# Kernel tuning notes

Hardware: AMD Instinct MI355X
Metric: run time of the kernel (lower is better)

Reference implementation:

```python
import jax, jax.numpy as jnp
import numpy as np

C_IN = 12      # total channels (rgb-noised + hidden)
C_NOISE = 3    # noise-prediction channels
HID = 128      # rule-MLP hidden size
PERC = 48      # perception channels (depthwise, 48/12 = 4 filters per channel)
TDIM = 256     # sinusoidal time-embedding dim


def setup_inputs() -> dict:
    key = jax.random.key(0)
    ks = jax.random.split(key, 12)
    B, H, W = 16, 256, 256
    x = jax.random.normal(ks[0], (B, C_NOISE, H, W), jnp.float32)
    hidden_channels = jax.random.normal(ks[1], (B, C_IN - C_NOISE, H, W), jnp.float32)
    t = jax.random.randint(ks[2], (B,), 0, 1000)
    # depthwise 3x3 perceive conv: torch weight shape [out=48, in/groups=1, 3, 3]
    w_perceive = jax.random.normal(ks[3], (PERC, 1, 3, 3), jnp.float32) * 0.1
    b_perceive = jax.random.normal(ks[4], (PERC,), jnp.float32) * 0.01
    # 1x1 convs of the rule network, stored as [out, in]
    w1 = jax.random.normal(ks[5], (HID, PERC), jnp.float32) * 0.1
    b1 = jax.random.normal(ks[6], (HID,), jnp.float32) * 0.01
    w2 = jax.random.normal(ks[7], (HID, HID), jnp.float32) * 0.05
    b2 = jax.random.normal(ks[8], (HID,), jnp.float32) * 0.01
    # conv3 is zero-initialized in the original; random here for test coverage
    w3 = jax.random.normal(ks[9], (C_IN, HID), jnp.float32) * 0.05
    # time embedding Linear(256 -> c_noise)
    w_time = jax.random.normal(ks[10], (C_NOISE, TDIM), jnp.float32) * 0.1
    b_time = jax.random.normal(ks[11], (C_NOISE,), jnp.float32) * 0.01
    return dict(x=x, hidden_channels=hidden_channels, t=t,
                w_perceive=w_perceive, b_perceive=b_perceive,
                w1=w1, b1=b1, w2=w2, b2=b2, w3=w3,
                w_time=w_time, b_time=b_time)


def _pos_encoding(t, channels):
    # t: [B] int -> [B, channels] sinusoidal embedding (torch repeat-then-scale layout)
    inv_freq = 1.0 / (10000.0 ** (jnp.arange(0, channels, 2, dtype=jnp.float32) / channels))
    ang = t.astype(jnp.float32)[:, None] * inv_freq  # [B, channels//2]
    return jnp.concatenate([jnp.sin(ang), jnp.cos(ang)], axis=-1)


def reference(x, hidden_channels, t, w_perceive, b_perceive, w1, b1, w2, b2, w3, w_time, b_time):
    # concat noised channels with hidden state channels -> [B, 12, H, W]
    xf = jnp.concatenate([x, hidden_channels], axis=1)
    # depthwise 3x3 conv, 'same' padding, groups = C_IN
    perc = jax.lax.conv_general_dilated(
        xf, w_perceive, window_strides=(1, 1), padding='SAME',
        feature_group_count=C_IN,
        dimension_numbers=('NCHW', 'OIHW', 'NCHW')) + b_perceive[None, :, None, None]
    # rule network: three 1x1 convs (pointwise MLP) with ReLUs
    h = jax.nn.relu(jnp.einsum('bchw,oc->bohw', perc, w1) + b1[None, :, None, None])
    h = jax.nn.relu(jnp.einsum('bchw,oc->bohw', h, w2) + b2[None, :, None, None])
    out = jnp.einsum('bchw,oc->bohw', h, w3)  # no bias
    # time embedding: sinusoidal -> SiLU -> Linear -> broadcast over H, W
    pe = _pos_encoding(t, TDIM)                       # [B, 256]
    emb = jax.nn.silu(pe) @ w_time.T + b_time         # [B, 3]
    noise_prediction = out[:, :C_NOISE] + emb[:, :, None, None]
    hidden_out = out[:, C_NOISE:]
    return (hidden_out, noise_prediction)
```

## Files before the change

### kernel.cpp

```cpp
#include <hip/hip_runtime.h>


#define ACT_S 136
#define PERC_S 72
#define NOISE_BASE 9437184

#define WSF_OFF 13312
#define WSF_BP 0
#define WSF_B1 48
#define WSF_B2 176
#define WSF_WP 304
#define WSF_EMB 736

typedef short bf16x8 __attribute__((ext_vector_type(8)));
typedef float f32x4 __attribute__((ext_vector_type(4)));

__device__ __forceinline__ short f2bf(float f) {
    union { float f; unsigned u; } cv; cv.f = f;
    unsigned r = cv.u + 0x7FFFu + ((cv.u >> 16) & 1u);
    return (short)(r >> 16);
}
__device__ __forceinline__ unsigned pk2bf(float f0, float f1) {
    union { float f; unsigned u; } a, b; a.f = f0; b.f = f1;
    return __builtin_amdgcn_perm(b.u + 0x8000u, a.u + 0x8000u, 0x07060302u);
}

__global__ void prep_emb_kernel(const float* __restrict__ wpg, const float* __restrict__ bpg,
                                const float* __restrict__ w1g, const float* __restrict__ b1g,
                                const float* __restrict__ w2g, const float* __restrict__ b2g,
                                const float* __restrict__ w3g,
                                const int* __restrict__ t,
                                const float* __restrict__ wt, const float* __restrict__ bt,
                                short* __restrict__ wsb, float* __restrict__ wsf)
{
    if (blockIdx.x < 107) {
        int i = blockIdx.x * 256 + threadIdx.x;
        if (i < 8192) {
            int o = i >> 6, c = i & 63;
            wsb[i] = (c < 48) ? f2bf(w1g[o * 48 + c]) : (short)0;
        } else if (i < 24576) {
            wsb[i] = f2bf(w2g[i - 8192]);
        } else if (i < 26624) {
            int k = i - 24576;
            wsb[i] = (k < 1536) ? f2bf(w3g[k]) : (short)0;
        } else if (i < 26672) {
            wsf[WSF_BP + (i - 26624)] = bpg[i - 26624];
        } else if (i < 26800) {
            wsf[WSF_B1 + (i - 26672)] = b1g[i - 26672];
        } else if (i < 26928) {
            wsf[WSF_B2 + (i - 26800)] = b2g[i - 26800];
        } else if (i < 27360) {
            wsf[WSF_WP + (i - 26928)] = wpg[i - 26928];
        }
        return;
    }
    int b = blockIdx.x - 107;
    int lane = threadIdx.x;
    if (lane >= 64) return;
    float tv = (float)t[b];
    float s0 = 0.f, s1 = 0.f, s2 = 0.f;
    const float LOG1E4 = 9.210340371976184f;
    #pragma unroll
    for (int ii = 0; ii < 2; ++ii) {
        int i = lane + ii * 64;
        float invf = __expf(-LOG1E4 * (float)i * (1.0f / 128.0f));
        float ang = tv * invf;
        float sn = sinf(ang), cs = cosf(ang);
        float ss = sn / (1.0f + __expf(-sn));
        float sc = cs / (1.0f + __expf(-cs));
        s0 += ss * wt[0 * 256 + i] + sc * wt[0 * 256 + i + 128];
        s1 += ss * wt[1 * 256 + i] + sc * wt[1 * 256 + i + 128];
        s2 += ss * wt[2 * 256 + i] + sc * wt[2 * 256 + i + 128];
    }
    #pragma unroll
    for (int off = 32; off; off >>= 1) {
        s0 += __shfl_down(s0, off);
        s1 += __shfl_down(s1, off);
        s2 += __shfl_down(s2, off);
    }
    if (lane == 0) {
        wsf[WSF_EMB + b * 3 + 0] = s0 + bt[0];
        wsf[WSF_EMB + b * 3 + 1] = s1 + bt[1];
        wsf[WSF_EMB + b * 3 + 2] = s2 + bt[2];
    }
}

__global__ __launch_bounds__(256, 3) void canet_main(
    const float* __restrict__ xg,
    const float* __restrict__ hg,
    const short* __restrict__ wsb,
    const float* __restrict__ wsf,
    float* __restrict__ outg)
{
    __shared__ __align__(16) short percS[64 * PERC_S];
    __shared__ __align__(16) short h1S[64 * ACT_S];
    __shared__ __align__(16) short h2S[64 * ACT_S];
    __shared__ __align__(16) float wp_s[48 * 12];
    __shared__ float bp_s[48];

    const int tid = threadIdx.x;
    const int b = blockIdx.x >> 8;
    const int y = blockIdx.x & 255;

    for (int i = tid; i < 576; i += 256) {
        int oc = i / 12, k = i % 12;
        wp_s[i] = (k < 9) ? wsf[WSF_WP + oc * 9 + k] : 0.0f;
    }
    if (tid < 48) bp_s[tid] = wsf[WSF_BP + tid];

    const int wv = tid >> 6;
    const int lane = tid & 63;
    const int m = lane & 15;
    const int q = lane >> 4;

    bf16x8 w1f[2][2], w2f[2][4], w3f[4];
    #pragma unroll
    for (int j = 0; j < 2; ++j) {
        int n = wv * 32 + j * 16 + m;
        #pragma unroll
        for (int ks = 0; ks < 2; ++ks)
            w1f[j][ks] = *(const bf16x8*)(wsb + n * 64 + ks * 32 + q * 8);
        #pragma unroll
        for (int ks = 0; ks < 4; ++ks)
            w2f[j][ks] = *(const bf16x8*)(wsb + 8192 + n * 128 + ks * 32 + q * 8);
    }
    #pragma unroll
    for (int ks = 0; ks < 4; ++ks)
        w3f[ks] = *(const bf16x8*)(wsb + 24576 + m * 128 + ks * 32 + q * 8);

    f32x4 b1v[2], b2v[2];
    #pragma unroll
    for (int j = 0; j < 2; ++j) {
        b1v[j] = *(const f32x4*)(wsf + WSF_B1 + wv * 32 + j * 16 + q * 4);
        b2v[j] = *(const f32x4*)(wsf + WSF_B2 + wv * 32 + j * 16 + q * 4);
    }
    const float embv = (m < 3) ? wsf[WSF_EMB + b * 3 + m] : 0.0f;

    const float* src3[3];
    #pragma unroll
    for (int i3 = 0; i3 < 3; ++i3) {
        int ic = 3 * q + i3;
        src3[i3] = (ic < 3) ? (xg + (((size_t)b * 3 + ic) << 16))
                            : (hg + (((size_t)b * 9 + (ic - 3)) << 16));
    }

    __syncthreads();

    for (int it = 0; it < 4; ++it) {
        const int x0 = it * 64;
        const int px = x0 + wv * 16 + m;

        {
            const int xm1 = px - (px > 0);
            const int xp1 = px + (px < 255);
            const bool okl = (px > 0), okr = (px < 255);
            short* prow = percS + (wv * 16 + m) * PERC_S;
            const bool interior = (y >= 1) && (y <= 254);
            #pragma unroll
            for (int i3 = 0; i3 < 3; ++i3) {
                const float* s = src3[i3];
                float tap[9];
                if (interior) {
                    #pragma unroll
                    for (int ky = 0; ky < 3; ++ky) {
                        const float* rp = s + (y + ky - 1) * 256;
                        float c0 = rp[xm1], c1 = rp[px], c2 = rp[xp1];
                        tap[ky * 3 + 0] = okl ? c0 : 0.0f;
                        tap[ky * 3 + 1] = c1;
                        tap[ky * 3 + 2] = okr ? c2 : 0.0f;
                    }
                } else {
                    #pragma unroll
                    for (int ky = 0; ky < 3; ++ky) {
                        int yy = y + ky - 1;
                        bool yok = (yy >= 0) && (yy < 256);
                        const float* rp = s + (yok ? yy : y) * 256;
                        float c0 = rp[xm1], c1 = rp[px], c2 = rp[xp1];
                        tap[ky * 3 + 0] = (yok && okl) ? c0 : 0.0f;
                        tap[ky * 3 + 1] = yok ? c1 : 0.0f;
                        tap[ky * 3 + 2] = (yok && okr) ? c2 : 0.0f;
                    }
                }
                float v[4];
                #pragma unroll
                for (int r = 0; r < 4; ++r) {
                    int oc = 12 * q + 4 * i3 + r;
                    const float* wrow = &wp_s[oc * 12];
                    f32x4 w0 = *(const f32x4*)wrow;
                    f32x4 w1_ = *(const f32x4*)(wrow + 4);
                    float a = bp_s[oc];
                    a += w0[0] * tap[0] + w0[1] * tap[1] + w0[2] * tap[2] + w0[3] * tap[3];
                    a += w1_[0] * tap[4] + w1_[1] * tap[5] + w1_[2] * tap[6] + w1_[3] * tap[7];
                    a += wrow[8] * tap[8];
                    v[r] = a;
                }
                uint2 pk;
                pk.x = pk2bf(v[0], v[1]);
                pk.y = pk2bf(v[2], v[3]);
                *(uint2*)(prow + 12 * q + 4 * i3) = pk;
            }
            *(uint2*)(prow + 48 + 4 * q) = uint2{0u, 0u};
        }
        __syncthreads();

        #pragma unroll
        for (int nt = 0; nt < 4; ++nt) {
            f32x4 c0 = b1v[0], c1 = b1v[1];
            #pragma unroll
            for (int ks = 0; ks < 2; ++ks) {
                bf16x8 p = *(const bf16x8*)(percS + (nt * 16 + m) * PERC_S + ks * 32 + q * 8);
                c0 = __builtin_amdgcn_mfma_f32_16x16x32_bf16(w1f[0][ks], p, c0, 0, 0, 0);
                c1 = __builtin_amdgcn_mfma_f32_16x16x32_bf16(w1f[1][ks], p, c1, 0, 0, 0);
            }
            short* drow = h1S + (nt * 16 + m) * ACT_S + wv * 32 + q * 4;
            uint2 pk;
            pk.x = pk2bf(fmaxf(c0[0], 0.f), fmaxf(c0[1], 0.f));
            pk.y = pk2bf(fmaxf(c0[2], 0.f), fmaxf(c0[3], 0.f));
            *(uint2*)drow = pk;
            pk.x = pk2bf(fmaxf(c1[0], 0.f), fmaxf(c1[1], 0.f));
            pk.y = pk2bf(fmaxf(c1[2], 0.f), fmaxf(c1[3], 0.f));
            *(uint2*)(drow + 16) = pk;
        }
        __syncthreads();

        #pragma unroll
        for (int nt = 0; nt < 4; ++nt) {
            f32x4 c0 = b2v[0], c1 = b2v[1];
            #pragma unroll
            for (int ks = 0; ks < 4; ++ks) {
                bf16x8 a = *(const bf16x8*)(h1S + (nt * 16 + m) * ACT_S + ks * 32 + q * 8);
                c0 = __builtin_amdgcn_mfma_f32_16x16x32_bf16(w2f[0][ks], a, c0, 0, 0, 0);
                c1 = __builtin_amdgcn_mfma_f32_16x16x32_bf16(w2f[1][ks], a, c1, 0, 0, 0);
            }
            short* drow = h2S + (nt * 16 + m) * ACT_S + wv * 32 + q * 4;
            uint2 pk;
            pk.x = pk2bf(fmaxf(c0[0], 0.f), fmaxf(c0[1], 0.f));
            pk.y = pk2bf(fmaxf(c0[2], 0.f), fmaxf(c0[3], 0.f));
            *(uint2*)drow = pk;
            pk.x = pk2bf(fmaxf(c1[0], 0.f), fmaxf(c1[1], 0.f));
            pk.y = pk2bf(fmaxf(c1[2], 0.f), fmaxf(c1[3], 0.f));
            *(uint2*)(drow + 16) = pk;
        }
        __syncthreads();

        {
            f32x4 acc = {0.f, 0.f, 0.f, 0.f};
            #pragma unroll
            for (int ks = 0; ks < 4; ++ks) {
                bf16x8 a = *(const bf16x8*)(h2S + (wv * 16 + m) * ACT_S + ks * 32 + q * 8);
                acc = __builtin_amdgcn_mfma_f32_16x16x32_bf16(a, w3f[ks], acc, 0, 0, 0);
            }
            if (m < 12) {
                int xx0 = x0 + wv * 16 + q * 4;
                size_t idx;
                if (m < 3) {
                    idx = (size_t)NOISE_BASE + (((size_t)b * 3 + m) << 16) + (size_t)y * 256 + xx0;
                } else {
                    idx = (((size_t)b * 9 + (m - 3)) << 16) + (size_t)y * 256 + xx0;
                }
                f32x4 vst = {acc[0] + embv, acc[1] + embv, acc[2] + embv, acc[3] + embv};
                *(f32x4*)(outg + idx) = vst;
            }
        }
    }
}

extern "C" void kernel_launch(void* const* d_in, const int* in_sizes, int n_in,
                              void* d_out, int out_size, void* d_ws, size_t ws_size,
                              hipStream_t stream) {
    const float* xg  = (const float*)d_in[0];
    const float* hg  = (const float*)d_in[1];
    const int*   tg  = (const int*)  d_in[2];
    const float* wpg = (const float*)d_in[3];
    const float* bpg = (const float*)d_in[4];
    const float* w1g = (const float*)d_in[5];
    const float* b1g = (const float*)d_in[6];
    const float* w2g = (const float*)d_in[7];
    const float* b2g = (const float*)d_in[8];
    const float* w3g = (const float*)d_in[9];
    const float* wtg = (const float*)d_in[10];
    const float* btg = (const float*)d_in[11];
    float* outg = (float*)d_out;
    short* wsb  = (short*)d_ws;
    float* wsf  = (float*)d_ws + WSF_OFF;

    prep_emb_kernel<<<123, 256, 0, stream>>>(wpg, bpg, w1g, b1g, w2g, b2g, w3g,
                                             tg, wtg, btg, wsb, wsf);
    canet_main<<<4096, 256, 0, stream>>>(xg, hg, wsb, wsf, outg);
}
```

Measured before the change: 226.8 us.

## Fold depthwise perceive conv into first MLP layer as MFMA over staged input taps

Precomputes a fused weight (w1 composed with the depthwise 3x3 filter) and fused bias in the prep kernel, so the first MLP layer becomes a K=144 (padded to 160) MFMA directly over a bf16 shared-memory tile of three input rows. This removes the per-pixel scalar FMA perception stage and its extra barrier, and loads the input rows once per block with coalesced float4 reads instead of scattered global taps. w2/w3 are now converted to bf16 inside the main kernel, block-to-row mapping is swizzled, and occupancy hint drops from 3 to 2 blocks. The cost is bf16 rounding of raw inputs, more MFMA work for layer 1, and larger LDS use.

```diff
diff --git a/kernel.cpp b/kernel.cpp
--- a/kernel.cpp
+++ b/kernel.cpp
@@ -2,15 +2,12 @@
 
 
 #define ACT_S 136
-#define PERC_S 72
+#define IN_ROW 4128
 #define NOISE_BASE 9437184
 
-#define WSF_OFF 13312
-#define WSF_BP 0
-#define WSF_B1 48
-#define WSF_B2 176
-#define WSF_WP 304
-#define WSF_EMB 736
+#define WSF_OFF 10240
+#define WSF_B1 0
+#define WSF_EMB 128
 
 typedef short bf16x8 __attribute__((ext_vector_type(8)));
 typedef float f32x4 __attribute__((ext_vector_type(4)));
@@ -20,41 +17,50 @@
     unsigned r = cv.u + 0x7FFFu + ((cv.u >> 16) & 1u);
     return (short)(r >> 16);
 }
+__device__ __forceinline__ short f2bf_fast(float f) {
+    union { float f; unsigned u; } cv; cv.f = f;
+    return (short)((cv.u + 0x8000u) >> 16);
+}
 __device__ __forceinline__ unsigned pk2bf(float f0, float f1) {
     union { float f; unsigned u; } a, b; a.f = f0; b.f = f1;
     return __builtin_amdgcn_perm(b.u + 0x8000u, a.u + 0x8000u, 0x07060302u);
 }
+__device__ __forceinline__ bf16x8 pk8bf(f32x4 a, f32x4 b) {
+    union { unsigned u[4]; bf16x8 v; } r;
+    r.u[0] = pk2bf(a[0], a[1]);
+    r.u[1] = pk2bf(a[2], a[3]);
+    r.u[2] = pk2bf(b[0], b[1]);
+    r.u[3] = pk2bf(b[2], b[3]);
+    return r.v;
+}
 
 __global__ void prep_emb_kernel(const float* __restrict__ wpg, const float* __restrict__ bpg,
                                 const float* __restrict__ w1g, const float* __restrict__ b1g,
-                                const float* __restrict__ w2g, const float* __restrict__ b2g,
-                                const float* __restrict__ w3g,
                                 const int* __restrict__ t,
                                 const float* __restrict__ wt, const float* __restrict__ bt,
                                 short* __restrict__ wsb, float* __restrict__ wsf)
 {
-    if (blockIdx.x < 107) {
+    if (blockIdx.x < 81) {
         int i = blockIdx.x * 256 + threadIdx.x;
-        if (i < 8192) {
-            int o = i >> 6, c = i & 63;
-            wsb[i] = (c < 48) ? f2bf(w1g[o * 48 + c]) : (short)0;
-        } else if (i < 24576) {
-            wsb[i] = f2bf(w2g[i - 8192]);
-        } else if (i < 26624) {
-            int k = i - 24576;
-            wsb[i] = (k < 1536) ? f2bf(w3g[k]) : (short)0;
-        } else if (i < 26672) {
-            wsf[WSF_BP + (i - 26624)] = bpg[i - 26624];
-        } else if (i < 26800) {
-            wsf[WSF_B1 + (i - 26672)] = b1g[i - 26672];
-        } else if (i < 26928) {
-            wsf[WSF_B2 + (i - 26800)] = b2g[i - 26800];
-        } else if (i < 27360) {
-            wsf[WSF_WP + (i - 26928)] = wpg[i - 26928];
+        if (i < 20480) {
+            int o = i / 160, k = i - o * 160;
+            int tp = k >> 4, icp = k & 15;
+            float val = 0.0f;
+            if (tp < 9 && icp < 12) {
+                #pragma unroll
+                for (int r = 0; r < 4; ++r)
+                    val += w1g[o * 48 + icp * 4 + r] * wpg[(icp * 4 + r) * 9 + tp];
+            }
+            wsb[i] = f2bf(val);
+        } else if (i < 20608) {
+            int o = i - 20480;
+            float v = b1g[o];
+            for (int oc = 0; oc < 48; ++oc) v += w1g[o * 48 + oc] * bpg[oc];
+            wsf[WSF_B1 + o] = v;
         }
         return;
     }
-    int b = blockIdx.x - 107;
+    int b = blockIdx.x - 81;
     int lane = threadIdx.x;
     if (lane >= 64) return;
     float tv = (float)t[b];
@@ -85,134 +91,119 @@
     }
 }
 
-__global__ __launch_bounds__(256, 3) void canet_main(
+__global__ __launch_bounds__(256, 2) void canet_main(
     const float* __restrict__ xg,
     const float* __restrict__ hg,
+    const float* __restrict__ w2g,
+    const float* __restrict__ b2g,
+    const float* __restrict__ w3g,
     const short* __restrict__ wsb,
     const float* __restrict__ wsf,
     float* __restrict__ outg)
 {
-    __shared__ __align__(16) short percS[64 * PERC_S];
+    __shared__ __align__(16) short inS[3 * IN_ROW];
     __shared__ __align__(16) short h1S[64 * ACT_S];
     __shared__ __align__(16) short h2S[64 * ACT_S];
-    __shared__ __align__(16) float wp_s[48 * 12];
-    __shared__ float bp_s[48];
 
     const int tid = threadIdx.x;
-    const int b = blockIdx.x >> 8;
-    const int y = blockIdx.x & 255;
-
-    for (int i = tid; i < 576; i += 256) {
-        int oc = i / 12, k = i % 12;
-        wp_s[i] = (k < 9) ? wsf[WSF_WP + oc * 9 + k] : 0.0f;
-    }
-    if (tid < 48) bp_s[tid] = wsf[WSF_BP + tid];
+    const int bid = blockIdx.x;
+    const int b = bid >> 8;
+    const int y = ((bid & 7) << 5) | ((bid >> 3) & 31);
+
+    for (int i = tid; i < 774; i += 256) {
+        int ky = i / 258, sx = i - ky * 258;
+        *(uint2*)(inS + ky * IN_ROW + sx * 16 + 12) = uint2{0u, 0u};
+    }
+    if (tid < 18) {
+        int ky = tid / 6, r2 = tid % 6;
+        int sx = (r2 & 1) ? 257 : 0, c4 = (r2 >> 1) * 4;
+        *(uint2*)(inS + ky * IN_ROW + sx * 16 + c4) = uint2{0u, 0u};
+    }
+
+    #pragma unroll
+    for (int s = 0; s < 9; ++s) {
+        int tk = tid + s * 256;
+        int ky = tk / 768;
+        int rem = tk - ky * 768;
+        int ch = rem >> 6;
+        int x = (rem & 63) << 2;
+        int yy = y + ky - 1;
+        float4 f = {0.f, 0.f, 0.f, 0.f};
+        if (yy >= 0 && yy < 256) {
+            const float* src = (ch < 3)
+                ? (xg + (((size_t)b * 3 + ch) << 16))
+                : (hg + (((size_t)b * 9 + (ch - 3)) << 16));
+            f = *(const float4*)(src + yy * 256 + x);
+        }
+        short* p = inS + ky * IN_ROW + (x + 1) * 16 + ch;
+        p[0]  = f2bf_fast(f.x);
+        p[16] = f2bf_fast(f.y);
+        p[32] = f2bf_fast(f.z);
+        p[48] = f2bf_fast(f.w);
+    }
 
     const int wv = tid >> 6;
     const int lane = tid & 63;
-    const int m = lane & 15;
+    const int i16 = lane & 15;
     const int q = lane >> 4;
-
-    bf16x8 w1f[2][2], w2f[2][4], w3f[4];
-    #pragma unroll
-    for (int j = 0; j < 2; ++j) {
-        int n = wv * 32 + j * 16 + m;
-        #pragma unroll
-        for (int ks = 0; ks < 2; ++ks)
-            w1f[j][ks] = *(const bf16x8*)(wsb + n * 64 + ks * 32 + q * 8);
-        #pragma unroll
-        for (int ks = 0; ks < 4; ++ks)
-            w2f[j][ks] = *(const bf16x8*)(wsb + 8192 + n * 128 + ks * 32 + q * 8);
-    }
-    #pragma unroll
-    for (int ks = 0; ks < 4; ++ks)
-        w3f[ks] = *(const bf16x8*)(wsb + 24576 + m * 128 + ks * 32 + q * 8);
+    const int qh = q >> 1;
+    const int hp = (q & 1) * 8;
+
+    bf16x8 w1f[2][5], w2f[2][4], w3f[4];
+    #pragma unroll
+    for (int jt = 0; jt < 2; ++jt) {
+        int o = wv * 32 + jt * 16 + i16;
+        #pragma unroll
+        for (int s = 0; s < 5; ++s)
+            w1f[jt][s] = *(const bf16x8*)(wsb + o * 160 + s * 32 + q * 8);
+        #pragma unroll
+        for (int ks = 0; ks < 4; ++ks) {
+            const float* wrow = w2g + o * 128 + ks * 32 + q * 8;
+            w2f[jt][ks] = pk8bf(*(const f32x4*)wrow, *(const f32x4*)(wrow + 4));
+        }
+    }
+    #pragma unroll
+    for (int ks = 0; ks < 4; ++ks) {
+        if (i16 < 12) {
+            const float* wrow = w3g + i16 * 128 + ks * 32 + q * 8;
+            w3f[ks] = pk8bf(*(const f32x4*)wrow, *(const f32x4*)(wrow + 4));
+        } else {
+            w3f[ks] = bf16x8{0, 0, 0, 0, 0, 0, 0, 0};
+        }
+    }
 
     f32x4 b1v[2], b2v[2];
     #pragma unroll
-    for (int j = 0; j < 2; ++j) {
-        b1v[j] = *(const f32x4*)(wsf + WSF_B1 + wv * 32 + j * 16 + q * 4);
-        b2v[j] = *(const f32x4*)(wsf + WSF_B2 + wv * 32 + j * 16 + q * 4);
-    }
-    const float embv = (m < 3) ? wsf[WSF_EMB + b * 3 + m] : 0.0f;
-
-    const float* src3[3];
-    #pragma unroll
-    for (int i3 = 0; i3 < 3; ++i3) {
-        int ic = 3 * q + i3;
-        src3[i3] = (ic < 3) ? (xg + (((size_t)b * 3 + ic) << 16))
-                            : (hg + (((size_t)b * 9 + (ic - 3)) << 16));
+    for (int jt = 0; jt < 2; ++jt) {
+        b1v[jt] = *(const f32x4*)(wsf + WSF_B1 + wv * 32 + jt * 16 + q * 4);
+        b2v[jt] = *(const f32x4*)(b2g + wv * 32 + jt * 16 + q * 4);
+    }
+    const float embv = (i16 < 3) ? wsf[WSF_EMB + b * 3 + i16] : 0.0f;
+
+    int vb[5];
+    #pragma unroll
+    for (int s = 0; s < 5; ++s) {
+        int tp = 2 * s + qh;
+        int ky, kx;
+        if (tp > 8) { ky = 0; kx = 0; }
+        else { ky = (tp * 11) >> 5; kx = tp - ky * 3; }
+        vb[s] = ky * IN_ROW + kx * 16 + hp + i16 * 16;
     }
 
     __syncthreads();
 
+    #pragma unroll
     for (int it = 0; it < 4; ++it) {
-        const int x0 = it * 64;
-        const int px = x0 + wv * 16 + m;
-
-        {
-            const int xm1 = px - (px > 0);
-            const int xp1 = px + (px < 255);
-            const bool okl = (px > 0), okr = (px < 255);
-            short* prow = percS + (wv * 16 + m) * PERC_S;
-            const bool interior = (y >= 1) && (y <= 254);
-            #pragma unroll
-            for (int i3 = 0; i3 < 3; ++i3) {
-                const float* s = src3[i3];
-                float tap[9];
-                if (interior) {
-                    #pragma unroll
-                    for (int ky = 0; ky < 3; ++ky) {
-                        const float* rp = s + (y + ky - 1) * 256;
-                        float c0 = rp[xm1], c1 = rp[px], c2 = rp[xp1];
-                        tap[ky * 3 + 0] = okl ? c0 : 0.0f;
-                        tap[ky * 3 + 1] = c1;
-                        tap[ky * 3 + 2] = okr ? c2 : 0.0f;
-                    }
-                } else {
-                    #pragma unroll
-                    for (int ky = 0; ky < 3; ++ky) {
-                        int yy = y + ky - 1;
-                        bool yok = (yy >= 0) && (yy < 256);
-                        const float* rp = s + (yok ? yy : y) * 256;
-                        float c0 = rp[xm1], c1 = rp[px], c2 = rp[xp1];
-                        tap[ky * 3 + 0] = (yok && okl) ? c0 : 0.0f;
-                        tap[ky * 3 + 1] = yok ? c1 : 0.0f;
-                        tap[ky * 3 + 2] = (yok && okr) ? c2 : 0.0f;
-                    }
-                }
-                float v[4];
-                #pragma unroll
-                for (int r = 0; r < 4; ++r) {
-                    int oc = 12 * q + 4 * i3 + r;
-                    const float* wrow = &wp_s[oc * 12];
-                    f32x4 w0 = *(const f32x4*)wrow;
-                    f32x4 w1_ = *(const f32x4*)(wrow + 4);
-                    float a = bp_s[oc];
-                    a += w0[0] * tap[0] + w0[1] * tap[1] + w0[2] * tap[2] + w0[3] * tap[3];
-                    a += w1_[0] * tap[4] + w1_[1] * tap[5] + w1_[2] * tap[6] + w1_[3] * tap[7];
-                    a += wrow[8] * tap[8];
-                    v[r] = a;
-                }
-                uint2 pk;
-                pk.x = pk2bf(v[0], v[1]);
-                pk.y = pk2bf(v[2], v[3]);
-                *(uint2*)(prow + 12 * q + 4 * i3) = pk;
-            }
-            *(uint2*)(prow + 48 + 4 * q) = uint2{0u, 0u};
-        }
-        __syncthreads();
-
         #pragma unroll
         for (int nt = 0; nt < 4; ++nt) {
             f32x4 c0 = b1v[0], c1 = b1v[1];
             #pragma unroll
-            for (int ks = 0; ks < 2; ++ks) {
-                bf16x8 p = *(const bf16x8*)(percS + (nt * 16 + m) * PERC_S + ks * 32 + q * 8);
-                c0 = __builtin_amdgcn_mfma_f32_16x16x32_bf16(w1f[0][ks], p, c0, 0, 0, 0);
-                c1 = __builtin_amdgcn_mfma_f32_16x16x32_bf16(w1f[1][ks], p, c1, 0, 0, 0);
-            }
-            short* drow = h1S + (nt * 16 + m) * ACT_S + wv * 32 + q * 4;
+            for (int s = 0; s < 5; ++s) {
+                bf16x8 p = *(const bf16x8*)(inS + vb[s] + (it * 64 + nt * 16) * 16);
+                c0 = __builtin_amdgcn_mfma_f32_16x16x32_bf16(w1f[0][s], p, c0, 0, 0, 0);
+                c1 = __builtin_amdgcn_mfma_f32_16x16x32_bf16(w1f[1][s], p, c1, 0, 0, 0);
+            }
+            short* drow = h1S + (nt * 16 + i16) * ACT_S + wv * 32 + q * 4;
             uint2 pk;
             pk.x = pk2bf(fmaxf(c0[0], 0.f), fmaxf(c0[1], 0.f));
             pk.y = pk2bf(fmaxf(c0[2], 0.f), fmaxf(c0[3], 0.f));
@@ -228,11 +219,11 @@
             f32x4 c0 = b2v[0], c1 = b2v[1];
             #pragma unroll
             for (int ks = 0; ks < 4; ++ks) {
-                bf16x8 a = *(const bf16x8*)(h1S + (nt * 16 + m) * ACT_S + ks * 32 + q * 8);
+                bf16x8 a = *(const bf16x8*)(h1S + (nt * 16 + i16) * ACT_S + ks * 32 + q * 8);
                 c0 = __builtin_amdgcn_mfma_f32_16x16x32_bf16(w2f[0][ks], a, c0, 0, 0, 0);
                 c1 = __builtin_amdgcn_mfma_f32_16x16x32_bf16(w2f[1][ks], a, c1, 0, 0, 0);
             }
-            short* drow = h2S + (nt * 16 + m) * ACT_S + wv * 32 + q * 4;
+            short* drow = h2S + (nt * 16 + i16) * ACT_S + wv * 32 + q * 4;
             uint2 pk;
             pk.x = pk2bf(fmaxf(c0[0], 0.f), fmaxf(c0[1], 0.f));
             pk.y = pk2bf(fmaxf(c0[2], 0.f), fmaxf(c0[3], 0.f));
@@ -247,16 +238,16 @@
             f32x4 acc = {0.f, 0.f, 0.f, 0.f};
             #pragma unroll
             for (int ks = 0; ks < 4; ++ks) {
-                bf16x8 a = *(const bf16x8*)(h2S + (wv * 16 + m) * ACT_S + ks * 32 + q * 8);
+                bf16x8 a = *(const bf16x8*)(h2S + (wv * 16 + i16) * ACT_S + ks * 32 + q * 8);
                 acc = __builtin_amdgcn_mfma_f32_16x16x32_bf16(a, w3f[ks], acc, 0, 0, 0);
             }
-            if (m < 12) {
-                int xx0 = x0 + wv * 16 + q * 4;
+            if (i16 < 12) {
+                int xx0 = it * 64 + wv * 16 + q * 4;
                 size_t idx;
-                if (m < 3) {
-                    idx = (size_t)NOISE_BASE + (((size_t)b * 3 + m) << 16) + (size_t)y * 256 + xx0;
+                if (i16 < 3) {
+                    idx = (size_t)NOISE_BASE + (((size_t)b * 3 + i16) << 16) + (size_t)y * 256 + xx0;
                 } else {
-                    idx = (((size_t)b * 9 + (m - 3)) << 16) + (size_t)y * 256 + xx0;
+                    idx = (((size_t)b * 9 + (i16 - 3)) << 16) + (size_t)y * 256 + xx0;
                 }
                 f32x4 vst = {acc[0] + embv, acc[1] + embv, acc[2] + embv, acc[3] + embv};
                 *(f32x4*)(outg + idx) = vst;
@@ -284,7 +275,7 @@
     short* wsb  = (short*)d_ws;
     float* wsf  = (float*)d_ws + WSF_OFF;
 
-    prep_emb_kernel<<<123, 256, 0, stream>>>(wpg, bpg, w1g, b1g, w2g, b2g, w3g,
-                                             tg, wtg, btg, wsb, wsf);
-    canet_main<<<4096, 256, 0, stream>>>(xg, hg, wsb, wsf, outg);
-}
+    prep_emb_kernel<<<97, 256, 0, stream>>>(wpg, bpg, w1g, b1g, tg, wtg, btg,
+                                            wsb, wsf);
+    canet_main<<<4096, 256, 0, stream>>>(xg, hg, w2g, b2g, w3g, wsb, wsf, outg);
+}
```

Result: slower. 253.6 us (+11.8%).
